# Kernel optimization log

Hardware: AMD Instinct MI355X
Metric: run time of the kernel (lower is better)

The kernel has to match this reference:

```python
import jax, jax.numpy as jnp
import numpy as np

N, S, C, P, K = 64, 64, 128, 32, 1000   # batch, frames, in_planes, part_num, class_num
HPG = (3 * C) // 16                      # hidden channels per group for part_score mlp = 24
EPS = 1e-5


def setup_inputs() -> dict:
    key = jax.random.key(0)
    ks = jax.random.split(key, 8)
    return {
        "t_f": jax.random.normal(ks[0], (N, S, C, P), jnp.float32),
        "t_s": jax.random.normal(ks[1], (N, S, C, P), jnp.float32),
        "t_l": jax.random.normal(ks[2], (N, S, C, P), jnp.float32),
        # part_score grouped 1x1 convs (groups=P): per-group (out, in)
        "w1": jax.random.normal(ks[3], (P, HPG, 3 * C), jnp.float32) * 0.05,
        "bn1_gamma": jnp.ones((P, HPG), jnp.float32),
        "bn1_beta": jnp.zeros((P, HPG), jnp.float32),
        "w2": jax.random.normal(ks[4], (P, 1, HPG), jnp.float32) * 0.05,
        # decay_channel grouped 1x1 conv: per-group 3C -> C
        "wd": jax.random.normal(ks[5], (P, C, 3 * C), jnp.float32) * 0.05,
        # per-part BatchNorm1d(C) affine params
        "bn_gamma": jnp.ones((P, C), jnp.float32),
        "bn_beta": jnp.zeros((P, C), jnp.float32),
        # fc: (1, C, K) in torch; squeeze leading 1
        "fc": jax.random.normal(ks[6], (C, K), jnp.float32) * 0.05,
    }


def reference(t_f, t_s, t_l, w1, bn1_gamma, bn1_beta, w2, wd, bn_gamma, bn_beta, fc):
    # cat along channel dim then arrange as (n, p, 3c, s) == grouped conv layout
    x = jnp.concatenate([t_f, t_s, t_l], axis=2).transpose(0, 3, 2, 1)  # (n,p,3c,s)

    # --- part_score: grouped 1x1 conv -> BN (batch stats over n,s) -> LeakyReLU -> grouped conv -> sigmoid
    h = jnp.einsum('npis,poi->npos', x, w1)               # (n,p,HPG,s)
    mu = h.mean(axis=(0, 3), keepdims=True)
    var = h.var(axis=(0, 3), keepdims=True)               # biased var (torch training BN)
    h = (h - mu) / jnp.sqrt(var + EPS) * bn1_gamma[None, :, :, None] + bn1_beta[None, :, :, None]
    h = jnp.where(h >= 0, h, 0.01 * h)                    # LeakyReLU(0.01)
    score = jax.nn.sigmoid(jnp.einsum('npis,poi->npos', h, w2))  # (n,p,1,s)

    # --- decay_channel grouped 1x1 conv: 3c -> c per part
    feat = jnp.einsum('npis,poi->npos', x, wd)            # (n,p,c,s)

    # attention-weighted temporal pooling
    wpv = (feat * score).sum(-1) / score.sum(-1)          # (n,p,c)

    # per-part BatchNorm1d over batch dim (training-mode batch stats)
    m = wpv.mean(axis=0)                                  # (p,c)
    v = wpv.var(axis=0)
    part_feature = ((wpv - m) / jnp.sqrt(v + EPS) * bn_gamma + bn_beta).transpose(1, 0, 2)  # (p,n,c)

    part_classification = jnp.einsum('pnc,ck->pnk', part_feature, fc)  # (p,n,K)

    # argmax frame per (n,p) and gather from t_f
    idx = jnp.argmax(score[:, :, 0, :], axis=-1)          # (n,p)
    tfp = t_f.transpose(0, 3, 1, 2)                       # (n,p,s,c)
    selected = jnp.take_along_axis(tfp, idx[:, :, None, None], axis=2)[:, :, 0, :]  # (n,p,c)
    selected_part_feature = selected.transpose(1, 0, 2)   # (p,n,c)

    weighted_part_vector = wpv.transpose(1, 0, 2)         # (p,n,c)
    return part_classification, weighted_part_vector, selected_part_feature
```

## Files before the change

### kernel.cpp

```cpp
#include <hip/hip_runtime.h>
#include <math.h>

#define N 64
#define S 64
#define C 128
#define P 32
#define KCLS 1000
#define HPG 24
#define C3 384
#define NS 4096
#define EPSV 1e-5f

#define WS_H    0
#define WS_W1Z  (WS_H + 2*P*HPG*NS)
#define WS_BNSS (WS_W1Z + 384*8*32*4)
#define WS_Y    (WS_BNSS + P*HPG*2)
#define WS_Z    (WS_Y + P*N*C3)
#define WS_PF   (WS_Z + P*N)
#define WS_SC   (WS_PF + P*C*N)
#define WS_MI   (WS_SC + N*P*S)

__global__ __launch_bounds__(256) void k0w_w1z(
    const float* __restrict__ w1, float* __restrict__ w1z)
{
  int e = blockIdx.x * 256 + threadIdx.x;
  int p = e & 31;
  int oq = (e >> 5) & 7;
  int i = e >> 8;
  float4 v;
  v.x = w1[(p * HPG + oq * 3 + 0) * C3 + i];
  v.y = w1[(p * HPG + oq * 3 + 1) * C3 + i];
  v.z = w1[(p * HPG + oq * 3 + 2) * C3 + i];
  v.w = 0.f;
  ((float4*)w1z)[e] = v;
}

__global__ __launch_bounds__(256) void k01_h(
    const float* __restrict__ tf, const float* __restrict__ ts,
    const float* __restrict__ tl, const float* __restrict__ w1z,
    float* __restrict__ h)
{
  int n = blockIdx.x, st = blockIdx.y, split = blockIdx.z;
  int s0 = st * 8;
  int t = threadIdx.x;
  int p = t & 31;
  int oq = t >> 5;
  __shared__ float xl[8192];
  float acc[3][8];
  #pragma unroll
  for (int oo = 0; oo < 3; ++oo)
    #pragma unroll
    for (int s = 0; s < 8; ++s) acc[oo][s] = 0.f;

  const float4* w4p = (const float4*)w1z;
  const float* srcs[3] = {tf, ts, tl};

  int aoff[8];
  int goff[8];
  #pragma unroll
  for (int j = 0; j < 8; ++j) {
    int a = (t + 256 * j) * 4;
    int c  = a >> 8;
    int sh = (a >> 7) & 1;
    int pp = (a >> 2) & 31;
    aoff[j] = a;
    goff[j] = sh * 4 * C * P + c * P + pp;
  }

  float4 stg[8];
  {
    int gch = split * 6;
    int z = gch >> 2, c0 = (gch & 3) * 32;
    const float* tb = srcs[z] + ((size_t)(n * S + s0)) * C * P + c0 * P;
    #pragma unroll
    for (int j = 0; j < 8; ++j) {
      const float* g = tb + goff[j];
      stg[j].x = g[0];
      stg[j].y = g[C * P];
      stg[j].z = g[2 * C * P];
      stg[j].w = g[3 * C * P];
    }
    #pragma unroll
    for (int j = 0; j < 8; ++j) *(float4*)&xl[aoff[j]] = stg[j];
  }
  __syncthreads();

  for (int ch = 0; ch < 6; ++ch) {
    if (ch < 5) {
      int gch2 = split * 6 + ch + 1;
      int z2 = gch2 >> 2, c02 = (gch2 & 3) * 32;
      const float* tb = srcs[z2] + ((size_t)(n * S + s0)) * C * P + c02 * P;
      #pragma unroll
      for (int j = 0; j < 8; ++j) {
        const float* g = tb + goff[j];
        stg[j].x = g[0];
        stg[j].y = g[C * P];
        stg[j].z = g[2 * C * P];
        stg[j].w = g[3 * C * P];
      }
    }
    int gch = split * 6 + ch;
    #pragma unroll 4
    for (int cl = 0; cl < 32; ++cl) {
      int i = gch * 32 + cl;
      float4 w  = w4p[(i * 8 + oq) * 32 + p];
      float4 x0 = *(const float4*)&xl[cl * 256 + p * 4];
      float4 x1 = *(const float4*)&xl[cl * 256 + 128 + p * 4];
      acc[0][0] += w.x * x0.x; acc[0][1] += w.x * x0.y;
      acc[0][2] += w.x * x0.z; acc[0][3] += w.x * x0.w;
      acc[0][4] += w.x * x1.x; acc[0][5] += w.x * x1.y;
      acc[0][6] += w.x * x1.z; acc[0][7] += w.x * x1.w;
      acc[1][0] += w.y * x0.x; acc[1][1] += w.y * x0.y;
      acc[1][2] += w.y * x0.z; acc[1][3] += w.y * x0.w;
      acc[1][4] += w.y * x1.x; acc[1][5] += w.y * x1.y;
      acc[1][6] += w.y * x1.z; acc[1][7] += w.y * x1.w;
      acc[2][0] += w.z * x0.x; acc[2][1] += w.z * x0.y;
      acc[2][2] += w.z * x0.z; acc[2][3] += w.z * x0.w;
      acc[2][4] += w.z * x1.x; acc[2][5] += w.z * x1.y;
      acc[2][6] += w.z * x1.z; acc[2][7] += w.z * x1.w;
    }
    __syncthreads();
    if (ch < 5) {
      #pragma unroll
      for (int j = 0; j < 8; ++j) *(float4*)&xl[aoff[j]] = stg[j];
      __syncthreads();
    }
  }

  #pragma unroll
  for (int oo = 0; oo < 3; ++oo) {
    int o = oq * 3 + oo;
    float* hp = h + ((size_t)split * P * HPG + p * HPG + o) * NS + n * S + s0;
    *(float4*)&hp[0] = make_float4(acc[oo][0], acc[oo][1], acc[oo][2], acc[oo][3]);
    *(float4*)&hp[4] = make_float4(acc[oo][4], acc[oo][5], acc[oo][6], acc[oo][7]);
  }
}

__global__ __launch_bounds__(256) void k2_bnstat(const float* __restrict__ h,
    const float* __restrict__ g, const float* __restrict__ b,
    float* __restrict__ bnss)
{
  int po = blockIdx.x;
  int t = threadIdx.x;
  const float4* r0 = (const float4*)(h + (size_t)po * NS);
  const float4* r1 = (const float4*)(h + (size_t)(P * HPG + po) * NS);
  float sm = 0.f, sq = 0.f;
  #pragma unroll
  for (int k = 0; k < 4; ++k) {
    float4 a = r0[t + 256 * k];
    float4 c = r1[t + 256 * k];
    float v0 = a.x + c.x, v1 = a.y + c.y, v2 = a.z + c.z, v3 = a.w + c.w;
    sm += v0 + v1 + v2 + v3;
    sq += v0 * v0 + v1 * v1 + v2 * v2 + v3 * v3;
  }
  #pragma unroll
  for (int m = 1; m < 64; m <<= 1) {
    sm += __shfl_xor(sm, m, 64);
    sq += __shfl_xor(sq, m, 64);
  }
  __shared__ float red[4][2];
  int w = t >> 6;
  if ((t & 63) == 0) { red[w][0] = sm; red[w][1] = sq; }
  __syncthreads();
  if (t == 0) {
    float sum = red[0][0] + red[1][0] + red[2][0] + red[3][0];
    float ssq = red[0][1] + red[1][1] + red[2][1] + red[3][1];
    float mu  = sum / (float)NS;
    float var = ssq / (float)NS - mu * mu;
    float sc = g[po] * rsqrtf(var + EPSV);
    bnss[po * 2]     = sc;
    bnss[po * 2 + 1] = b[po] - mu * sc;
  }
}

__global__ __launch_bounds__(256) void k3a_score(
    const float* __restrict__ h, const float* __restrict__ bnss,
    const float* __restrict__ w2,
    float* __restrict__ score, float* __restrict__ z,
    int* __restrict__ mi_out)
{
  int n = blockIdx.x;
  int p = blockIdx.y * 4 + (threadIdx.x >> 6);
  int l = threadIdx.x & 63;
  float ssum = 0.f;
  const float* hp0 = h + (size_t)p * HPG * NS + n * S;
  const float* hp1 = hp0 + (size_t)P * HPG * NS;
  #pragma unroll
  for (int o = 0; o < HPG; ++o) {
    float hv = hp0[(size_t)o * NS + l] + hp1[(size_t)o * NS + l];
    float sc = bnss[(p * HPG + o) * 2];
    float sh = bnss[(p * HPG + o) * 2 + 1];
    float v = hv * sc + sh;
    v = (v >= 0.f) ? v : 0.01f * v;
    ssum += w2[p * HPG + o] * v;
  }
  float scr = 1.f / (1.f + expf(-ssum));
  float zs = scr;
  #pragma unroll
  for (int m = 1; m < 64; m <<= 1) zs += __shfl_xor(zs, m, 64);
  float mv = scr; int mi = l;
  #pragma unroll
  for (int m = 1; m < 64; m <<= 1) {
    float ov = __shfl_xor(mv, m, 64);
    int   oi = __shfl_xor(mi, m, 64);
    if (ov > mv || (ov == mv && oi < mi)) { mv = ov; mi = oi; }
  }
  if (l == 0) { z[p * N + n] = zs; mi_out[n * P + p] = mi; }
  score[((size_t)n * P + p) * S + l] = scr;
}

__global__ __launch_bounds__(256) void k3b_y(
    const float* __restrict__ tf, const float* __restrict__ ts,
    const float* __restrict__ tl, const float* __restrict__ score,
    const int* __restrict__ mi, float* __restrict__ y,
    float* __restrict__ out_spf)
{
  int n = blockIdx.x, chunk = blockIdx.y;
  int z = chunk >> 2, c0 = (chunk & 3) * 32;
  const float* src = (z == 0) ? tf : (z == 1) ? ts : tl;
  int t = threadIdx.x;
  int p = t & 31, cl = t >> 5;
  __shared__ float sc_lds[S * P];
  __shared__ int mi_lds[P];
  #pragma unroll
  for (int j = 0; j < 8; ++j) {
    int e = t + 256 * j;
    int s2 = e >> 5, pp = e & 31;
    sc_lds[s2 * P + pp] = score[((size_t)n * P + pp) * S + s2];
  }
  if (t < P) mi_lds[t] = mi[n * P + t];
  __syncthreads();
  int mymi = mi_lds[p];
  const float* base = src + (size_t)n * S * C * P + (size_t)(c0 + cl) * P + p;
  float acc[4] = {0.f, 0.f, 0.f, 0.f};
  float sel[4] = {0.f, 0.f, 0.f, 0.f};
  #pragma unroll 8
  for (int s = 0; s < S; ++s) {
    float scv = sc_lds[s * P + p];
    #pragma unroll
    for (int j = 0; j < 4; ++j) {
      float v = base[(size_t)s * C * P + j * 8 * P];
      acc[j] += v * scv;
      sel[j] = (s == mymi) ? v : sel[j];
    }
  }
  float* yp = y + ((size_t)p * N + n) * C3 + z * C + c0 + cl;
  #pragma unroll
  for (int j = 0; j < 4; ++j) yp[j * 8] = acc[j];
  if (z == 0) {
    float* sp = out_spf + ((size_t)p * N + n) * C + c0 + cl;
    #pragma unroll
    for (int j = 0; j < 4; ++j) sp[j * 8] = sel[j];
  }
}

__global__ __launch_bounds__(256) void k4_wpv(
    const float* __restrict__ y, const float* __restrict__ z,
    const float* __restrict__ wd, const float* __restrict__ g,
    const float* __restrict__ b, float* __restrict__ out_wpv,
    float* __restrict__ pf)
{
  int p   = blockIdx.x;
  int cch = blockIdx.y;
  int t = threadIdx.x;
  int n = t & 63, cg = t >> 6;
  int cbase = cch * 16 + cg * 4;
  __shared__ float ych[96][66];
  float acc[4] = {0.f, 0.f, 0.f, 0.f};
  const float* yp  = y  + (size_t)p * N * C3;
  const float* wdp = wd + (size_t)p * C * C3;
  for (int ch = 0; ch < 4; ++ch) {
    __syncthreads();
    #pragma unroll
    for (int j = 0; j < 24; ++j) {
      int e = t + 256 * j;
      int i = e % 96, nn = e / 96;
      ych[i][nn] = yp[nn * C3 + ch * 96 + i];
    }
    __syncthreads();
    #pragma unroll
    for (int sub = 0; sub < 4; ++sub) {
      float yr[24];
      #pragma unroll
      for (int kk = 0; kk < 24; ++kk) yr[kk] = ych[sub * 24 + kk][n];
      int ibase = ch * 96 + sub * 24;
      #pragma unroll
      for (int cl = 0; cl < 4; ++cl) {
        const float4* w4 = (const float4*)(wdp + (size_t)(cbase + cl) * C3 + ibase);
        float a = 0.f;
        #pragma unroll
        for (int q = 0; q < 6; ++q) {
          float4 wv = w4[q];
          a += yr[q*4+0] * wv.x + yr[q*4+1] * wv.y
             + yr[q*4+2] * wv.z + yr[q*4+3] * wv.w;
        }
        acc[cl] += a;
      }
    }
  }
  float zinv = 1.f / z[p * N + n];
  #pragma unroll
  for (int cl = 0; cl < 4; ++cl) acc[cl] *= zinv;
  #pragma unroll
  for (int cl = 0; cl < 4; ++cl) {
    float v = acc[cl];
    float s = v, q = v * v;
    #pragma unroll
    for (int m = 1; m < 64; m <<= 1) {
      s += __shfl_xor(s, m, 64);
      q += __shfl_xor(q, m, 64);
    }
    float mu  = s * (1.f / 64.f);
    float var = q * (1.f / 64.f) - mu * mu;
    int c = cbase + cl;
    float sc = g[p * C + c] * rsqrtf(var + EPSV);
    float sh = b[p * C + c] - mu * sc;
    pf[((size_t)p * C + c) * N + n] = v * sc + sh;
  }
  float4 wout = make_float4(acc[0], acc[1], acc[2], acc[3]);
  *(float4*)(out_wpv + ((size_t)p * N + n) * C + cbase) = wout;
}

__global__ __launch_bounds__(256) void k5_fc(
    const float* __restrict__ pf, const float* __restrict__ fc,
    float* __restrict__ out0)
{
  int kt = blockIdx.x;
  int p  = blockIdx.y;
  int n0 = blockIdx.z * 16;
  int t = threadIdx.x;
  int k = kt * 256 + t;
  bool ok = k < KCLS;
  int kk = ok ? k : (KCLS - 1);
  float acc[16];
  #pragma unroll
  for (int j = 0; j < 16; ++j) acc[j] = 0.f;
  for (int c = 0; c < C; ++c) {
    float fv = fc[c * KCLS + kk];
    const float4* row4 = (const float4*)(pf + ((size_t)p * C + c) * N + n0);
    #pragma unroll
    for (int j4 = 0; j4 < 4; ++j4) {
      float4 r = row4[j4];
      acc[j4*4+0] += r.x * fv; acc[j4*4+1] += r.y * fv;
      acc[j4*4+2] += r.z * fv; acc[j4*4+3] += r.w * fv;
    }
  }
  if (ok) {
    #pragma unroll 4
    for (int j = 0; j < 16; ++j)
      out0[(size_t)(p * N + n0 + j) * KCLS + k] = acc[j];
  }
}

extern "C" void kernel_launch(void* const* d_in, const int* in_sizes, int n_in,
                              void* d_out, int out_size, void* d_ws, size_t ws_size,
                              hipStream_t stream)
{
  const float* tf = (const float*)d_in[0];
  const float* ts = (const float*)d_in[1];
  const float* tl = (const float*)d_in[2];
  const float* w1 = (const float*)d_in[3];
  const float* g1 = (const float*)d_in[4];
  const float* b1 = (const float*)d_in[5];
  const float* w2 = (const float*)d_in[6];
  const float* wd = (const float*)d_in[7];
  const float* g  = (const float*)d_in[8];
  const float* b  = (const float*)d_in[9];
  const float* fc = (const float*)d_in[10];

  float* ws   = (float*)d_ws;
  float* h    = ws + WS_H;
  float* w1z  = ws + WS_W1Z;
  float* bnss = ws + WS_BNSS;
  float* y    = ws + WS_Y;
  float* z    = ws + WS_Z;
  float* pf   = ws + WS_PF;
  float* sc   = ws + WS_SC;
  int*   mi   = (int*)(ws + WS_MI);

  float* out0 = (float*)d_out;
  float* out1 = out0 + P * N * KCLS;
  float* out2 = out1 + P * N * C;

  k0w_w1z<<<384, 256, 0, stream>>>(w1, w1z);
  k01_h<<<dim3(64, 8, 2), 256, 0, stream>>>(tf, ts, tl, w1z, h);
  k2_bnstat<<<768, 256, 0, stream>>>(h, g1, b1, bnss);
  k3a_score<<<dim3(64, 8), 256, 0, stream>>>(h, bnss, w2, sc, z, mi);
  k3b_y<<<dim3(64, 12), 256, 0, stream>>>(tf, ts, tl, sc, mi, y, out2);
  k4_wpv<<<dim3(32, 8), 256, 0, stream>>>(y, z, wd, g, b, out1, pf);
  k5_fc<<<dim3(4, 32, 4), 256, 0, stream>>>(pf, fc, out0);
}
```

Before: 160.1 us.

## Split input channels across half-waves with six outputs per thread in h conv

Reorganizes the grouped 1x1 conv kernel so each thread computes six hidden outputs over half of the input channels instead of three outputs over all of them. The two half-wave partials are combined with a cross-lane shuffle, and only one half writes. The weight layout is repacked to 8-float records, so each shared-memory x load now feeds more FMAs and the zero padding per output drops. In exchange it needs more accumulator registers and adds a shuffle reduction.

```diff
diff --git a/kernel.cpp b/kernel.cpp
--- a/kernel.cpp
+++ b/kernel.cpp
@@ -13,7 +13,7 @@
 
 #define WS_H    0
 #define WS_W1Z  (WS_H + 2*P*HPG*NS)
-#define WS_BNSS (WS_W1Z + 384*8*32*4)
+#define WS_BNSS (WS_W1Z + 384*4*32*8)
 #define WS_Y    (WS_BNSS + P*HPG*2)
 #define WS_Z    (WS_Y + P*N*C3)
 #define WS_PF   (WS_Z + P*N)
@@ -21,38 +21,45 @@
 #define WS_MI   (WS_SC + N*P*S)
 
 __global__ __launch_bounds__(256) void k0w_w1z(
-    const float* __restrict__ w1, float* __restrict__ w1z)
+    const float* __restrict__ w1, float* __restrict__ w8)
 {
   int e = blockIdx.x * 256 + threadIdx.x;
-  int p = e & 31;
-  int oq = (e >> 5) & 7;
+  int half = e & 1;
+  int p = (e >> 1) & 31;
+  int oh = (e >> 6) & 3;
   int i = e >> 8;
   float4 v;
-  v.x = w1[(p * HPG + oq * 3 + 0) * C3 + i];
-  v.y = w1[(p * HPG + oq * 3 + 1) * C3 + i];
-  v.z = w1[(p * HPG + oq * 3 + 2) * C3 + i];
-  v.w = 0.f;
-  ((float4*)w1z)[e] = v;
+  if (half == 0) {
+    v.x = w1[(p * HPG + oh * 6 + 0) * C3 + i];
+    v.y = w1[(p * HPG + oh * 6 + 1) * C3 + i];
+    v.z = w1[(p * HPG + oh * 6 + 2) * C3 + i];
+    v.w = w1[(p * HPG + oh * 6 + 3) * C3 + i];
+  } else {
+    v.x = w1[(p * HPG + oh * 6 + 4) * C3 + i];
+    v.y = w1[(p * HPG + oh * 6 + 5) * C3 + i];
+    v.z = 0.f; v.w = 0.f;
+  }
+  ((float4*)w8)[e] = v;
 }
 
 __global__ __launch_bounds__(256) void k01_h(
     const float* __restrict__ tf, const float* __restrict__ ts,
-    const float* __restrict__ tl, const float* __restrict__ w1z,
+    const float* __restrict__ tl, const float* __restrict__ w8,
     float* __restrict__ h)
 {
   int n = blockIdx.x, st = blockIdx.y, split = blockIdx.z;
   int s0 = st * 8;
   int t = threadIdx.x;
   int p = t & 31;
-  int oq = t >> 5;
+  int ih = (t >> 5) & 1;
+  int oh = t >> 6;
   __shared__ float xl[8192];
-  float acc[3][8];
-  #pragma unroll
-  for (int oo = 0; oo < 3; ++oo)
+  float acc[6][8];
+  #pragma unroll
+  for (int oo = 0; oo < 6; ++oo)
     #pragma unroll
     for (int s = 0; s < 8; ++s) acc[oo][s] = 0.f;
 
-  const float4* w4p = (const float4*)w1z;
   const float* srcs[3] = {tf, ts, tl};
 
   int aoff[8];
@@ -101,23 +108,24 @@
     }
     int gch = split * 6 + ch;
     #pragma unroll 4
-    for (int cl = 0; cl < 32; ++cl) {
+    for (int k = 0; k < 16; ++k) {
+      int cl = ih * 16 + k;
       int i = gch * 32 + cl;
-      float4 w  = w4p[(i * 8 + oq) * 32 + p];
+      const float* wb = w8 + ((size_t)(i * 4 + oh) * 32 + p) * 8;
+      float4 wA = *(const float4*)wb;
+      float2 wB = *(const float2*)(wb + 4);
       float4 x0 = *(const float4*)&xl[cl * 256 + p * 4];
       float4 x1 = *(const float4*)&xl[cl * 256 + 128 + p * 4];
-      acc[0][0] += w.x * x0.x; acc[0][1] += w.x * x0.y;
-      acc[0][2] += w.x * x0.z; acc[0][3] += w.x * x0.w;
-      acc[0][4] += w.x * x1.x; acc[0][5] += w.x * x1.y;
-      acc[0][6] += w.x * x1.z; acc[0][7] += w.x * x1.w;
-      acc[1][0] += w.y * x0.x; acc[1][1] += w.y * x0.y;
-      acc[1][2] += w.y * x0.z; acc[1][3] += w.y * x0.w;
-      acc[1][4] += w.y * x1.x; acc[1][5] += w.y * x1.y;
-      acc[1][6] += w.y * x1.z; acc[1][7] += w.y * x1.w;
-      acc[2][0] += w.z * x0.x; acc[2][1] += w.z * x0.y;
-      acc[2][2] += w.z * x0.z; acc[2][3] += w.z * x0.w;
-      acc[2][4] += w.z * x1.x; acc[2][5] += w.z * x1.y;
-      acc[2][6] += w.z * x1.z; acc[2][7] += w.z * x1.w;
+      float xs[8] = {x0.x, x0.y, x0.z, x0.w, x1.x, x1.y, x1.z, x1.w};
+      #pragma unroll
+      for (int ss = 0; ss < 8; ++ss) {
+        acc[0][ss] += wA.x * xs[ss];
+        acc[1][ss] += wA.y * xs[ss];
+        acc[2][ss] += wA.z * xs[ss];
+        acc[3][ss] += wA.w * xs[ss];
+        acc[4][ss] += wB.x * xs[ss];
+        acc[5][ss] += wB.y * xs[ss];
+      }
     }
     __syncthreads();
     if (ch < 5) {
@@ -128,11 +136,19 @@
   }
 
   #pragma unroll
-  for (int oo = 0; oo < 3; ++oo) {
-    int o = oq * 3 + oo;
-    float* hp = h + ((size_t)split * P * HPG + p * HPG + o) * NS + n * S + s0;
-    *(float4*)&hp[0] = make_float4(acc[oo][0], acc[oo][1], acc[oo][2], acc[oo][3]);
-    *(float4*)&hp[4] = make_float4(acc[oo][4], acc[oo][5], acc[oo][6], acc[oo][7]);
+  for (int oo = 0; oo < 6; ++oo)
+    #pragma unroll
+    for (int ss = 0; ss < 8; ++ss)
+      acc[oo][ss] += __shfl_xor(acc[oo][ss], 32, 64);
+
+  if (ih == 0) {
+    #pragma unroll
+    for (int oo = 0; oo < 6; ++oo) {
+      int o = oh * 6 + oo;
+      float* hp = h + ((size_t)split * P * HPG + p * HPG + o) * NS + n * S + s0;
+      *(float4*)&hp[0] = make_float4(acc[oo][0], acc[oo][1], acc[oo][2], acc[oo][3]);
+      *(float4*)&hp[4] = make_float4(acc[oo][4], acc[oo][5], acc[oo][6], acc[oo][7]);
+    }
   }
 }
 
@@ -370,7 +386,7 @@
 
   float* ws   = (float*)d_ws;
   float* h    = ws + WS_H;
-  float* w1z  = ws + WS_W1Z;
+  float* w8   = ws + WS_W1Z;
   float* bnss = ws + WS_BNSS;
   float* y    = ws + WS_Y;
   float* z    = ws + WS_Z;
@@ -382,8 +398,8 @@
   float* out1 = out0 + P * N * KCLS;
   float* out2 = out1 + P * N * C;
 
-  k0w_w1z<<<384, 256, 0, stream>>>(w1, w1z);
-  k01_h<<<dim3(64, 8, 2), 256, 0, stream>>>(tf, ts, tl, w1z, h);
+  k0w_w1z<<<384, 256, 0, stream>>>(w1, w8);
+  k01_h<<<dim3(64, 8, 2), 256, 0, stream>>>(tf, ts, tl, w8, h);
   k2_bnstat<<<768, 256, 0, stream>>>(h, g1, b1, bnss);
   k3a_score<<<dim3(64, 8), 256, 0, stream>>>(h, bnss, w2, sc, z, mi);
   k3b_y<<<dim3(64, 12), 256, 0, stream>>>(tf, ts, tl, sc, mi, y, out2);
```

Result: slower. 174.0 us (+8.6%).
